# Kernel optimization log

Measured on AMD Instinct MI355X. Metric: run time of the kernel, lower is better.

## Reference

```python
import jax, jax.numpy as jnp
from jax import lax
import numpy as np

B, S, D, STEPS = 16, 2048, 1024, 50

def setup_inputs() -> dict:
    key = jax.random.key(0)
    k1, k2, k3, k4 = jax.random.split(key, 4)
    latent = jax.random.normal(k1, (B, S, D), dtype=jnp.float32)
    W = jax.random.normal(k2, (D, 3), dtype=jnp.float32) * (1.0 / np.sqrt(D))
    b = jax.random.normal(k3, (3,), dtype=jnp.float32) * 0.02
    noise = jax.random.normal(k4, (B, S, 3), dtype=jnp.float32)
    return {"latent": latent, "W": W, "b": b, "noise": noise, "steps": STEPS}


def reference(latent, W, b, noise, steps):
    # target = coord_proj(latent)
    target = jnp.einsum("bsd,dc->bsc", latent, W) + b  # [B,S,3]
    # loop t = steps-1 .. 0, alpha = (t+1)/steps  ->  alphas = steps/steps, ..., 1/steps
    alphas = (jnp.arange(steps, 0, -1).astype(target.dtype)) / jnp.asarray(steps, target.dtype)
    def step(x, a):
        return a * x + (1.0 - a) * target, None
    x, _ = lax.scan(step, noise, alphas)
    return x
```

## Files before the change

kernel.cpp:

```cpp
#include <hip/hip_runtime.h>


#define D_DIM 1024
#define NCHUNK (D_DIM / 256)

__launch_bounds__(256, 4)
__global__ void diffusion_init_kernel(const float* __restrict__ latent,
                                      const float* __restrict__ W,
                                      const float* __restrict__ bias,
                                      const float* __restrict__ noise,
                                      const int* __restrict__ steps_p,
                                      float* __restrict__ out,
                                      int rows) {
    const int lane   = threadIdx.x & 63;
    const int wid    = (blockIdx.x * blockDim.x + threadIdx.x) >> 6;
    const int nwaves = (gridDim.x * blockDim.x) >> 6;

    int steps = steps_p[0];
    if (steps <= 0 || steps > (1 << 20)) {
        float fs = __int_as_float(steps);
        if (fs >= 1.0f && fs < 1.0e6f) steps = (int)(fs + 0.5f);
        else steps = 50;
    }
    double pd = 1.0;
    for (int t = 1; t <= steps; ++t) pd *= (double)t / (double)steps;
    const float P   = (float)pd;
    const float omP = (float)(1.0 - pd);

    float wv[NCHUNK][12];
    const float4* W4 = (const float4*)W;
    #pragma unroll
    for (int j = 0; j < NCHUNK; ++j) {
        #pragma unroll
        for (int q = 0; q < 3; ++q) {
            float4 t = W4[j * 192 + lane * 3 + q];
            wv[j][q * 4 + 0] = t.x;
            wv[j][q * 4 + 1] = t.y;
            wv[j][q * 4 + 2] = t.z;
            wv[j][q * 4 + 3] = t.w;
        }
    }
    const float b0 = bias[0], b1 = bias[1], b2 = bias[2];

    const float4* L4 = (const float4*)latent;
    for (int row = wid; row < rows; row += nwaves) {
        float a0 = 0.f, a1 = 0.f, a2 = 0.f;
        const size_t rb = (size_t)row * (D_DIM / 4);
        #pragma unroll
        for (int j = 0; j < NCHUNK; ++j) {
            float4 v = L4[rb + j * 64 + lane];
            a0 = fmaf(v.x, wv[j][0], a0);
            a1 = fmaf(v.x, wv[j][1], a1);
            a2 = fmaf(v.x, wv[j][2], a2);
            a0 = fmaf(v.y, wv[j][3], a0);
            a1 = fmaf(v.y, wv[j][4], a1);
            a2 = fmaf(v.y, wv[j][5], a2);
            a0 = fmaf(v.z, wv[j][6], a0);
            a1 = fmaf(v.z, wv[j][7], a1);
            a2 = fmaf(v.z, wv[j][8], a2);
            a0 = fmaf(v.w, wv[j][9], a0);
            a1 = fmaf(v.w, wv[j][10], a1);
            a2 = fmaf(v.w, wv[j][11], a2);
        }
        #pragma unroll
        for (int off = 32; off > 0; off >>= 1) {
            a0 += __shfl_xor(a0, off, 64);
            a1 += __shfl_xor(a1, off, 64);
            a2 += __shfl_xor(a2, off, 64);
        }
        if (lane == 0) {
            const size_t o = (size_t)row * 3;
            out[o + 0] = omP * (a0 + b0) + P * noise[o + 0];
            out[o + 1] = omP * (a1 + b1) + P * noise[o + 1];
            out[o + 2] = omP * (a2 + b2) + P * noise[o + 2];
        }
    }
}

extern "C" void kernel_launch(void* const* d_in, const int* in_sizes, int n_in,
                              void* d_out, int out_size, void* d_ws, size_t ws_size,
                              hipStream_t stream) {
    const float* latent = (const float*)d_in[0];
    const float* W      = (const float*)d_in[1];
    const float* bias   = (const float*)d_in[2];
    const float* noise  = (const float*)d_in[3];
    const int*   steps  = (const int*)d_in[4];
    float* out = (float*)d_out;

    const int rows = in_sizes[3] / 3;

    const int blocks = 2048;
    diffusion_init_kernel<<<blocks, 256, 0, stream>>>(latent, W, bias, noise,
                                                      steps, out, rows);
}
```

Measured before the change: 32.32 us.

## Stage weights in LDS, batch nontemporal latent loads, and compute decay factor in log space

Projection weights now live in shared memory instead of 48 registers per lane, which is meant to cut register pressure so the launch bound can allow 8 blocks per SIMD. All four latent chunks are issued up front as nontemporal loads to raise memory-level parallelism. The output write is spread across three lanes, each with a prefetched noise value. The fp64 product loop is replaced by a float log2 sum, which is cheaper but slightly less precise and caps at 2048 terms.

```diff
diff --git a/kernel.cpp b/kernel.cpp
--- a/kernel.cpp
+++ b/kernel.cpp
@@ -4,7 +4,9 @@
 #define D_DIM 1024
 #define NCHUNK (D_DIM / 256)
 
-__launch_bounds__(256, 4)
+typedef float floatx4 __attribute__((ext_vector_type(4)));
+
+__launch_bounds__(256, 8)
 __global__ void diffusion_init_kernel(const float* __restrict__ latent,
                                       const float* __restrict__ W,
                                       const float* __restrict__ bias,
@@ -16,63 +18,76 @@
     const int wid    = (blockIdx.x * blockDim.x + threadIdx.x) >> 6;
     const int nwaves = (gridDim.x * blockDim.x) >> 6;
 
+    __shared__ float wlds[D_DIM * 3];
+    {
+        const floatx4* Wg = (const floatx4*)W;
+        floatx4*       Ws = (floatx4*)wlds;
+        #pragma unroll
+        for (int i = 0; i < 3; ++i)
+            Ws[threadIdx.x + i * 256] = Wg[threadIdx.x + i * 256];
+    }
+    __syncthreads();
+
+    const float bl = bias[lane < 3 ? lane : 0];
+
     int steps = steps_p[0];
     if (steps <= 0 || steps > (1 << 20)) {
         float fs = __int_as_float(steps);
-        if (fs >= 1.0f && fs < 1.0e6f) steps = (int)(fs + 0.5f);
-        else steps = 50;
+        steps = (fs >= 1.0f && fs < 1.0e6f) ? (int)(fs + 0.5f) : 50;
     }
-    double pd = 1.0;
-    for (int t = 1; t <= steps; ++t) pd *= (double)t / (double)steps;
-    const float P   = (float)pd;
-    const float omP = (float)(1.0 - pd);
+    const int ntp = steps < 2048 ? steps : 2048;
+    float logp = 0.f;
+    const float ls = __log2f((float)steps);
+    for (int t = 1; t <= ntp; ++t) logp += __log2f((float)t) - ls;
+    const float P   = exp2f(logp);
+    const float omP = 1.0f - P;
 
-    float wv[NCHUNK][12];
-    const float4* W4 = (const float4*)W;
-    #pragma unroll
-    for (int j = 0; j < NCHUNK; ++j) {
-        #pragma unroll
-        for (int q = 0; q < 3; ++q) {
-            float4 t = W4[j * 192 + lane * 3 + q];
-            wv[j][q * 4 + 0] = t.x;
-            wv[j][q * 4 + 1] = t.y;
-            wv[j][q * 4 + 2] = t.z;
-            wv[j][q * 4 + 3] = t.w;
-        }
-    }
-    const float b0 = bias[0], b1 = bias[1], b2 = bias[2];
+    const floatx4* L4 = (const floatx4*)latent;
+    const floatx4* WL = (const floatx4*)wlds;
 
-    const float4* L4 = (const float4*)latent;
     for (int row = wid; row < rows; row += nwaves) {
-        float a0 = 0.f, a1 = 0.f, a2 = 0.f;
+        const size_t o = (size_t)row * 3;
+        float nv = 0.f;
+        if (lane < 3) nv = noise[o + lane];
+
+        floatx4 cur[NCHUNK];
         const size_t rb = (size_t)row * (D_DIM / 4);
         #pragma unroll
+        for (int j = 0; j < NCHUNK; ++j)
+            cur[j] = __builtin_nontemporal_load(&L4[rb + j * 64 + lane]);
+
+        float a0 = 0.f, a1 = 0.f, a2 = 0.f;
+        #pragma unroll
         for (int j = 0; j < NCHUNK; ++j) {
-            float4 v = L4[rb + j * 64 + lane];
-            a0 = fmaf(v.x, wv[j][0], a0);
-            a1 = fmaf(v.x, wv[j][1], a1);
-            a2 = fmaf(v.x, wv[j][2], a2);
-            a0 = fmaf(v.y, wv[j][3], a0);
-            a1 = fmaf(v.y, wv[j][4], a1);
-            a2 = fmaf(v.y, wv[j][5], a2);
-            a0 = fmaf(v.z, wv[j][6], a0);
-            a1 = fmaf(v.z, wv[j][7], a1);
-            a2 = fmaf(v.z, wv[j][8], a2);
-            a0 = fmaf(v.w, wv[j][9], a0);
-            a1 = fmaf(v.w, wv[j][10], a1);
-            a2 = fmaf(v.w, wv[j][11], a2);
+            const floatx4 w0 = WL[j * 192 + lane * 3 + 0];
+            const floatx4 w1 = WL[j * 192 + lane * 3 + 1];
+            const floatx4 w2 = WL[j * 192 + lane * 3 + 2];
+            const floatx4 t  = cur[j];
+            a0 = fmaf(t.x, w0.x, a0);
+            a1 = fmaf(t.x, w0.y, a1);
+            a2 = fmaf(t.x, w0.z, a2);
+            a0 = fmaf(t.y, w0.w, a0);
+            a1 = fmaf(t.y, w1.x, a1);
+            a2 = fmaf(t.y, w1.y, a2);
+            a0 = fmaf(t.z, w1.z, a0);
+            a1 = fmaf(t.z, w1.w, a1);
+            a2 = fmaf(t.z, w2.x, a2);
+            a0 = fmaf(t.w, w2.y, a0);
+            a1 = fmaf(t.w, w2.z, a1);
+            a2 = fmaf(t.w, w2.w, a2);
         }
+
         #pragma unroll
         for (int off = 32; off > 0; off >>= 1) {
             a0 += __shfl_xor(a0, off, 64);
             a1 += __shfl_xor(a1, off, 64);
             a2 += __shfl_xor(a2, off, 64);
         }
-        if (lane == 0) {
-            const size_t o = (size_t)row * 3;
-            out[o + 0] = omP * (a0 + b0) + P * noise[o + 0];
-            out[o + 1] = omP * (a1 + b1) + P * noise[o + 1];
-            out[o + 2] = omP * (a2 + b2) + P * noise[o + 2];
+
+        if (lane < 3) {
+            const float sl = lane == 0 ? a0 : lane == 1 ? a1 : a2;
+            __builtin_nontemporal_store(omP * (sl + bl) + P * nv,
+                                        &out[o + lane]);
         }
     }
 }
```

Measured after the change: 40.48 us. 1.25x slower.
